# Performance work log

Measured on AMD Instinct MI355X. Metric: run time of the kernel, lower is better.

Reference implementation:

```python
import jax, jax.numpy as jnp
import numpy as np

LAMBDA_COLOR = 0.01
BLUR = 0.01          # geomloss blur
P = 2                # geomloss p
EPS_FINAL = BLUR ** P  # 1e-4
# Note: with scaling=1.2 (>1), geomloss's epsilon_schedule arange is empty, so
# eps_list = [diameter**p, blur**p] -> exactly two annealing stages.


def cost_matrix(x, y, lambda_color):
    # x: [B,N,6], y: [B,M,6]
    cx, col_x = x[..., :3], x[..., 3:]
    cy, col_y = y[..., :3], y[..., 3:]
    max_norm = jnp.max(jnp.linalg.norm(jnp.concatenate([cx, cy], axis=1), axis=-1))
    s = 1.0 / (max_norm + 1e-6)
    cxn, cyn = cx * s, cy * s
    coord = jnp.sum((cxn[:, :, None, :] - cyn[:, None, :, :]) ** 2, axis=-1)  # [B,N,M]
    col_x = jnp.clip(col_x, 0.0, 1.0)
    col_y = jnp.clip(col_y, 0.0, 1.0)
    col = jnp.sum((col_x[:, :, None, :] - col_y[:, None, :, :]) ** 2, axis=-1)
    return jnp.maximum(coord + lambda_color * col, 0.0)


def softmin(eps, C, h):
    # h: [B,M] = log_weights + potential/eps ; C: [B,N,M]
    return -eps * jax.nn.logsumexp(h[:, None, :] - C / eps, axis=2)  # [B,N]


def sinkhorn_distance(x, y, lambda_color):
    B, N, _ = x.shape
    M = y.shape[1]
    a_log = jnp.full((B, N), -np.log(N), dtype=x.dtype)
    b_log = jnp.full((B, M), -np.log(M), dtype=x.dtype)

    C_xy = cost_matrix(x, y, lambda_color)          # [B,N,M]
    C_yx = jnp.swapaxes(C_xy, 1, 2)                 # cost is symmetric in x<->y

    # diameter over raw 6-d features (geomloss max_diameter)
    pts = jnp.concatenate([x.reshape(-1, x.shape[-1]), y.reshape(-1, y.shape[-1])], axis=0)
    diameter = jnp.linalg.norm(pts.max(0) - pts.min(0))
    eps_list = (diameter ** P, jnp.asarray(EPS_FINAL, x.dtype))

    # Sinkhorn loop runs without gradient through the potentials (geomloss semantics)
    Cs_xy = jax.lax.stop_gradient(C_xy)
    Cs_yx = jax.lax.stop_gradient(C_yx)

    eps = eps_list[0]
    f = softmin(eps, Cs_xy, b_log)   # potential on x
    g = softmin(eps, Cs_yx, a_log)   # potential on y
    for eps in eps_list:
        ft = softmin(eps, Cs_xy, b_log + g / eps)
        gt = softmin(eps, Cs_yx, a_log + f / eps)
        f, g = 0.5 * (f + ft), 0.5 * (g + gt)

    # final extrapolation with gradient-carrying cost, detached dual potentials
    eps = eps_list[-1]
    f_new = softmin(eps, C_xy, b_log + jax.lax.stop_gradient(g) / eps)
    g_new = softmin(eps, C_yx, a_log + jax.lax.stop_gradient(f) / eps)

    # <a,f> + <b,g> with uniform weights
    ot = f_new.mean(axis=1) + g_new.mean(axis=1)   # [B]
    return ot.mean() * 10.0


def setup_inputs() -> dict:
    key = jax.random.key(0)
    kx, ky = jax.random.split(key)
    x = jax.random.normal(kx, (4, 4096, 6), dtype=jnp.float32)
    y = jax.random.normal(ky, (4, 4096, 6), dtype=jnp.float32)
    return {"x": x, "y": y}


def reference(x, y):
    return sinkhorn_distance(x, y, LAMBDA_COLOR)
```

## Files before the change

### kernel.cpp

```cpp
#include <hip/hip_runtime.h>

#define B_ 4
#define N_ 4096
#define ROWS (B_ * N_)
#define PTS_TOTAL (2 * ROWS)

#define LOG2E 1.4426950408889634f
#define LN2   0.6931471805599453f
#define EPS1  1e-4f
#define NEG_LOG2M (-12.0f)
#define EPS1LNM 8.317766166719343e-4f
#define ENC_STRIDE 32

typedef _Float16 h2 __attribute__((ext_vector_type(2)));
typedef _Float16 v8h __attribute__((ext_vector_type(8)));
typedef float f32x4 __attribute__((ext_vector_type(4)));

__device__ inline float fexp2(float x) { return __builtin_amdgcn_exp2f(x); }
__device__ inline float flog2(float x) { return __builtin_amdgcn_logf(x); }

__device__ inline unsigned fenc(float f) {
  unsigned u = __float_as_uint(f);
  return (u & 0x80000000u) ? ~u : (u | 0x80000000u);
}
__device__ inline float fdec(unsigned u) {
  return (u & 0x80000000u) ? __uint_as_float(u & 0x7fffffffu)
                           : __uint_as_float(~u);
}
__device__ inline unsigned pkh2(float a, float b) {
  h2 hv; hv.x = (_Float16)a; hv.y = (_Float16)b;
  return __builtin_bit_cast(unsigned, hv);
}
__device__ inline v8h bcv8(uint4 u) { return __builtin_bit_cast(v8h, u); }

__global__ void init_kernel(unsigned* enc, float* MOM) {
  int t = threadIdx.x;
  if (t < 13) enc[t * ENC_STRIDE] = 0u;
  if (t < 512) MOM[t] = 0.0f;
}

__global__ __launch_bounds__(256) void reduce_kernel(
    const float* __restrict__ x, const float* __restrict__ y,
    unsigned* __restrict__ enc) {
  int idx = blockIdx.x * 256 + threadIdx.x;
  bool isx = idx < ROWS;
  const float* p = (isx ? x : y) + (size_t)(isx ? idx : idx - ROWS) * 6;
  float d[6];
#pragma unroll
  for (int k = 0; k < 6; ++k) d[k] = p[k];
  unsigned e[13];
  e[0] = fenc(d[0] * d[0] + d[1] * d[1] + d[2] * d[2]);
#pragma unroll
  for (int k = 0; k < 6; ++k) {
    e[1 + k] = fenc(d[k]);
    e[7 + k] = fenc(-d[k]);
  }
#pragma unroll
  for (int off = 32; off > 0; off >>= 1) {
#pragma unroll
    for (int k = 0; k < 13; ++k) {
      unsigned o = (unsigned)__shfl_xor((int)e[k], off);
      e[k] = e[k] > o ? e[k] : o;
    }
  }
  __shared__ unsigned sh[4][13];
  int wave = threadIdx.x >> 6, lane = threadIdx.x & 63;
  if (lane == 0) {
#pragma unroll
    for (int k = 0; k < 13; ++k) sh[wave][k] = e[k];
  }
  __syncthreads();
  if (threadIdx.x < 13) {
    unsigned v = sh[0][threadIdx.x];
#pragma unroll
    for (int w = 1; w < 4; ++w) v = v > sh[w][threadIdx.x] ? v : sh[w][threadIdx.x];
    atomicMax(&enc[threadIdx.x * ENC_STRIDE], v);
  }
}

__global__ __launch_bounds__(256) void pack_kernel(
    const float* __restrict__ x, const float* __restrict__ y,
    float4* __restrict__ XP, uint4* __restrict__ AREC,
    uint4* __restrict__ BREC, const unsigned* __restrict__ enc,
    float* __restrict__ sc, float* __restrict__ MOM1) {
  int g = blockIdx.x * 256 + threadIdx.x;
  int side = g >> 14, local = g & (ROWS - 1), batch = local >> 12;
  float s = 1.0f / (sqrtf(fdec(enc[0])) + 1e-6f);
  float eps0 = 0.0f;
#pragma unroll
  for (int k = 0; k < 6; ++k) {
    float dd = fdec(enc[(1 + k) * ENC_STRIDE]) + fdec(enc[(7 + k) * ENC_STRIDE]);
    eps0 += dd * dd;
  }
  if (g == 0) sc[0] = eps0;

  const float* p = (side ? y : x) + (size_t)local * 6;
  float v[6];
  v[0] = p[0] * s; v[1] = p[1] * s; v[2] = p[2] * s;
  v[3] = 0.1f * fminf(fmaxf(p[3], 0.0f), 1.0f);
  v[4] = 0.1f * fminf(fmaxf(p[4], 0.0f), 1.0f);
  v[5] = 0.1f * fminf(fmaxf(p[5], 0.0f), 1.0f);
  float q = v[0]*v[0] + v[1]*v[1] + v[2]*v[2] + v[3]*v[3] + v[4]*v[4] + v[5]*v[5];
  XP[(size_t)g * 2]     = make_float4(v[0], v[1], v[2], v[3]);
  XP[(size_t)g * 2 + 1] = make_float4(v[4], v[5], q, 0.0f);
  unsigned w01 = pkh2(v[0], v[1]), w23 = pkh2(v[2], v[3]), w45 = pkh2(v[4], v[5]);
  AREC[g] = (uint4){w01, w23, w45, pkh2(1.0f, 0.0f)};
  BREC[g] = (uint4){w01, w23, w45, 0u};

  float w = fexp2(NEG_LOG2M - q * (LOG2E / eps0));
  float acc[28];
  acc[0] = w;
  int kk = 1;
#pragma unroll
  for (int d = 0; d < 6; ++d) acc[kk++] = w * v[d];
#pragma unroll
  for (int d = 0; d < 6; ++d) {
    float wv = w * v[d];
#pragma unroll
    for (int e = d; e < 6; ++e) acc[kk++] = wv * v[e];
  }
#pragma unroll
  for (int off = 32; off > 0; off >>= 1) {
#pragma unroll
    for (int k = 0; k < 28; ++k) acc[k] += __shfl_xor(acc[k], off);
  }
  __shared__ float sh[4][28];
  int wave = threadIdx.x >> 6, lane = threadIdx.x & 63;
  if (lane == 0) {
#pragma unroll
    for (int k = 0; k < 28; ++k) sh[wave][k] = acc[k];
  }
  __syncthreads();
  if (threadIdx.x < 28) {
    float vv = (sh[0][threadIdx.x] + sh[1][threadIdx.x]) +
               (sh[2][threadIdx.x] + sh[3][threadIdx.x]);
    atomicAdd(&MOM1[(side * 4 + batch) * 32 + threadIdx.x], vv);
  }
}

__device__ inline float taylor_f(const float* __restrict__ M, const float* v,
                                 float q, float eps0) {
  float sc2 = 2.0f * LOG2E / eps0;
  float p[6];
#pragma unroll
  for (int d = 0; d < 6; ++d) p[d] = v[d] * sc2;
  float t1 = 0.0f;
#pragma unroll
  for (int d = 0; d < 6; ++d) t1 += p[d] * M[1 + d];
  float t2 = 0.0f;
  int kk = 7;
#pragma unroll
  for (int d = 0; d < 6; ++d) {
#pragma unroll
    for (int e = d; e < 6; ++e) {
      float coef = (d == e) ? 1.0f : 2.0f;
      t2 += coef * p[d] * p[e] * M[kk];
      kk++;
    }
  }
  float S = M[0] + LN2 * t1 + (0.5f * LN2 * LN2) * t2;
  return q - eps0 * LN2 * flog2(S);
}

__global__ __launch_bounds__(256) void rows1_kernel(
    const float4* __restrict__ XP, const float* __restrict__ MOM1,
    float* __restrict__ MOM2, float* __restrict__ FG1,
    const float* __restrict__ sc) {
  int g = blockIdx.x * 256 + threadIdx.x;
  int side = g >> 14, local = g & (ROWS - 1), batch = local >> 12;
  float eps0 = sc[0];
  float4 a = XP[(size_t)g * 2], b = XP[(size_t)g * 2 + 1];
  float v[6] = {a.x, a.y, a.z, a.w, b.x, b.y};
  float q = b.z;
  const float* M = MOM1 + (((side ^ 1) * 4 + batch) * 32);
  float f1 = taylor_f(M, v, q, eps0);
  FG1[g] = f1;
  float w = fexp2(NEG_LOG2M + (f1 - q) * (LOG2E / eps0));
  float acc[28];
  acc[0] = w;
  int kk = 1;
#pragma unroll
  for (int d = 0; d < 6; ++d) acc[kk++] = w * v[d];
#pragma unroll
  for (int d = 0; d < 6; ++d) {
    float wv = w * v[d];
#pragma unroll
    for (int e = d; e < 6; ++e) acc[kk++] = wv * v[e];
  }
#pragma unroll
  for (int off = 32; off > 0; off >>= 1) {
#pragma unroll
    for (int k = 0; k < 28; ++k) acc[k] += __shfl_xor(acc[k], off);
  }
  __shared__ float sh[4][28];
  int wave = threadIdx.x >> 6, lane = threadIdx.x & 63;
  if (lane == 0) {
#pragma unroll
    for (int k = 0; k < 28; ++k) sh[wave][k] = acc[k];
  }
  __syncthreads();
  if (threadIdx.x < 28) {
    float vv = (sh[0][threadIdx.x] + sh[1][threadIdx.x]) +
               (sh[2][threadIdx.x] + sh[3][threadIdx.x]);
    atomicAdd(&MOM2[(side * 4 + batch) * 32 + threadIdx.x], vv);
  }
}

__global__ __launch_bounds__(256) void rows2_kernel(
    const float4* __restrict__ XP, const float* __restrict__ MOM2,
    const float* __restrict__ FG1, float* __restrict__ FG2,
    unsigned* __restrict__ BRECu, const float* __restrict__ sc) {
  int g = blockIdx.x * 256 + threadIdx.x;
  int side = g >> 14, local = g & (ROWS - 1), batch = local >> 12;
  float eps0 = sc[0];
  float4 a = XP[(size_t)g * 2], b = XP[(size_t)g * 2 + 1];
  float v[6] = {a.x, a.y, a.z, a.w, b.x, b.y};
  float q = b.z;
  const float* M = MOM2 + (((side ^ 1) * 4 + batch) * 32);
  float f_t = taylor_f(M, v, q, eps0);
  float f2v = 0.5f * (FG1[g] + f_t);
  FG2[g] = f2v;
  float hs2 = 0.5f * (f2v - q - EPS1LNM);
  BRECu[4 * g + 3] = pkh2(hs2, 0.0f);
}

__global__ __launch_bounds__(256) void softmax_pair_kernel(
    const uint4* __restrict__ AREC, const uint4* __restrict__ BIN,
    uint4* __restrict__ BOUT, const float* __restrict__ XPf,
    const float* __restrict__ prev, float* __restrict__ part) {
  int t = threadIdx.x;
  int wave = t >> 6, lane = t & 63;
  int l16 = lane & 15;
  bool ld = lane < 16;
  int grow0 = blockIdx.x * 32;
  int side = grow0 >> 14;
  int batch = (grow0 & (ROWS - 1)) >> 12;
  int colrec0 = (side ^ 1) * ROWS + batch * 4096 + wave * 1024;

  uint4 z4 = (uint4){0u, 0u, 0u, 0u};
  uint4 a1u = z4, a2u = z4;
  if (ld) {
    a1u = AREC[grow0 + l16];
    a2u = AREC[grow0 + 16 + l16];
  }
  v8h a1 = bcv8(a1u), a2 = bcv8(a2u);

  f32x4 m2a = {-3.0e38f, -3.0e38f, -3.0e38f, -3.0e38f};
  f32x4 m2b = m2a;
  const f32x4 cz = {0.0f, 0.0f, 0.0f, 0.0f};

#pragma unroll 4
  for (int tt = 0; tt < 64; ++tt) {
    uint4 bu = z4;
    if (ld) bu = BIN[colrec0 + tt * 16 + l16];
    v8h b = bcv8(bu);
    f32x4 d1 = __builtin_amdgcn_mfma_f32_16x16x32_f16(a1, b, cz, 0, 0, 0);
    f32x4 d2 = __builtin_amdgcn_mfma_f32_16x16x32_f16(a2, b, cz, 0, 0, 0);
    m2a = __builtin_elementwise_max(m2a, d1);
    m2b = __builtin_elementwise_max(m2b, d2);
  }

#pragma unroll
  for (int off = 1; off <= 8; off <<= 1) {
#pragma unroll
    for (int r = 0; r < 4; ++r) {
      m2a[r] = fmaxf(m2a[r], __shfl_xor(m2a[r], off));
      m2b[r] = fmaxf(m2b[r], __shfl_xor(m2b[r], off));
    }
  }

  __shared__ float lm[4][32];
  __shared__ float fsh[32];
  if (l16 == 0) {
    int qd = lane >> 4;
#pragma unroll
    for (int r = 0; r < 4; ++r) {
      lm[wave][qd * 4 + r] = m2a[r];
      lm[wave][16 + qd * 4 + r] = m2b[r];
    }
  }
  __syncthreads();
  if (t < 32) {
    int g = grow0 + t;
    float m = fmaxf(fmaxf(lm[0][t], lm[1][t]), fmaxf(lm[2][t], lm[3][t]));
    float q = XPf[(size_t)g * 8 + 6];
    float f_t = q - 2.0f * m;
    float fo = prev ? 0.5f * (prev[g] + f_t) : f_t;
    if (BOUT) {
      float hs = 0.5f * (fo - q - EPS1LNM);
      uint4 ar = AREC[g];
      BOUT[g] = (uint4){ar.x, ar.y, ar.z, pkh2(hs, 0.0f)};
    }
    if (part) {
      fsh[t] = fo;
      __builtin_amdgcn_s_waitcnt(0);
      if (t == 0) {
        float ssum = 0.0f;
#pragma unroll
        for (int k = 0; k < 32; ++k) ssum += fsh[k];
        part[blockIdx.x] = ssum;
      }
    }
  }
}

__global__ __launch_bounds__(256) void final_kernel(
    const float* __restrict__ part, float* __restrict__ out) {
  float acc = 0.0f;
  for (int i = threadIdx.x; i < 1024; i += 256) acc += part[i];
  __shared__ float sh[256];
  sh[threadIdx.x] = acc;
  __syncthreads();
  for (int st = 128; st > 0; st >>= 1) {
    if (threadIdx.x < st) sh[threadIdx.x] += sh[threadIdx.x + st];
    __syncthreads();
  }
  if (threadIdx.x == 0) out[0] = sh[0] * (10.0f / (float)ROWS);
}

extern "C" void kernel_launch(void* const* d_in, const int* in_sizes, int n_in,
                              void* d_out, int out_size, void* d_ws,
                              size_t ws_size, hipStream_t stream) {
  const float* x = (const float*)d_in[0];
  const float* y = (const float*)d_in[1];
  float* out = (float*)d_out;
  float* w = (float*)d_ws;
  unsigned* enc = (unsigned*)d_ws;
  float* sc   = w + 448;
  float* MOM  = w + 512;
  float* MOM1 = MOM;
  float* MOM2 = MOM + 256;
  float* base = w + 1024;
  float4* XP   = (float4*)base;
  uint4* AREC  = (uint4*)(base + 262144);
  uint4* BRECA = (uint4*)(base + 262144 + 131072);
  uint4* BRECB = (uint4*)(base + 262144 + 262144);
  float* FG1   = base + 262144 + 262144 + 131072;
  float* FG2   = FG1 + PTS_TOTAL;
  float* PART  = FG2 + PTS_TOTAL;

  init_kernel<<<1, 512, 0, stream>>>(enc, MOM);
  reduce_kernel<<<PTS_TOTAL / 256, 256, 0, stream>>>(x, y, enc);
  pack_kernel<<<PTS_TOTAL / 256, 256, 0, stream>>>(x, y, XP, AREC, BRECA, enc,
                                                   sc, MOM1);
  rows1_kernel<<<PTS_TOTAL / 256, 256, 0, stream>>>(XP, MOM1, MOM2, FG1, sc);
  rows2_kernel<<<PTS_TOTAL / 256, 256, 0, stream>>>(XP, MOM2, FG1, FG2,
                                                    (unsigned*)BRECA, sc);
  softmax_pair_kernel<<<1024, 256, 0, stream>>>(AREC, BRECA, BRECB,
                                                (const float*)XP, FG2, nullptr);
  softmax_pair_kernel<<<1024, 256, 0, stream>>>(AREC, BRECB, nullptr,
                                                (const float*)XP, nullptr, PART);
  final_kernel<<<1, 256, 0, stream>>>(PART, out);
}
```

Baseline: 118.0 us.

## Fuse all stages into one persistent kernel with software grid barriers

Replaces the chain of eight kernel launches with one 256-block persistent kernel that separates stages with atomic-counter grid barriers. Global max and moment reductions now go through per-block partial buffers, with no atomics into shared accumulators. Each block handles 128 rows and reuses 8 A fragments per B load in the MFMA max loop. The final sum is accumulated into the output by atomics. This removes launch overhead and intermediate buffers (XP, FG1/FG2). It assumes all 256 blocks are co-resident and spin-waits at each barrier, and the softmax phase now runs on only 256 blocks instead of 1024.

```diff
diff --git a/kernel.cpp b/kernel.cpp
--- a/kernel.cpp
+++ b/kernel.cpp
@@ -1,16 +1,13 @@
 #include <hip/hip_runtime.h>
 
-#define B_ 4
-#define N_ 4096
-#define ROWS (B_ * N_)
-#define PTS_TOTAL (2 * ROWS)
+#define ROWS 16384
+#define PTS_TOTAL 32768
+#define NBLK 256
 
 #define LOG2E 1.4426950408889634f
 #define LN2   0.6931471805599453f
-#define EPS1  1e-4f
 #define NEG_LOG2M (-12.0f)
 #define EPS1LNM 8.317766166719343e-4f
-#define ENC_STRIDE 32
 
 typedef _Float16 h2 __attribute__((ext_vector_type(2)));
 typedef _Float16 v8h __attribute__((ext_vector_type(8)));
@@ -18,128 +15,14 @@
 
 __device__ inline float fexp2(float x) { return __builtin_amdgcn_exp2f(x); }
 __device__ inline float flog2(float x) { return __builtin_amdgcn_logf(x); }
-
-__device__ inline unsigned fenc(float f) {
-  unsigned u = __float_as_uint(f);
-  return (u & 0x80000000u) ? ~u : (u | 0x80000000u);
-}
-__device__ inline float fdec(unsigned u) {
-  return (u & 0x80000000u) ? __uint_as_float(u & 0x7fffffffu)
-                           : __uint_as_float(~u);
-}
 __device__ inline unsigned pkh2(float a, float b) {
   h2 hv; hv.x = (_Float16)a; hv.y = (_Float16)b;
   return __builtin_bit_cast(unsigned, hv);
 }
 __device__ inline v8h bcv8(uint4 u) { return __builtin_bit_cast(v8h, u); }
 
-__global__ void init_kernel(unsigned* enc, float* MOM) {
-  int t = threadIdx.x;
-  if (t < 13) enc[t * ENC_STRIDE] = 0u;
-  if (t < 512) MOM[t] = 0.0f;
-}
-
-__global__ __launch_bounds__(256) void reduce_kernel(
-    const float* __restrict__ x, const float* __restrict__ y,
-    unsigned* __restrict__ enc) {
-  int idx = blockIdx.x * 256 + threadIdx.x;
-  bool isx = idx < ROWS;
-  const float* p = (isx ? x : y) + (size_t)(isx ? idx : idx - ROWS) * 6;
-  float d[6];
-#pragma unroll
-  for (int k = 0; k < 6; ++k) d[k] = p[k];
-  unsigned e[13];
-  e[0] = fenc(d[0] * d[0] + d[1] * d[1] + d[2] * d[2]);
-#pragma unroll
-  for (int k = 0; k < 6; ++k) {
-    e[1 + k] = fenc(d[k]);
-    e[7 + k] = fenc(-d[k]);
-  }
-#pragma unroll
-  for (int off = 32; off > 0; off >>= 1) {
-#pragma unroll
-    for (int k = 0; k < 13; ++k) {
-      unsigned o = (unsigned)__shfl_xor((int)e[k], off);
-      e[k] = e[k] > o ? e[k] : o;
-    }
-  }
-  __shared__ unsigned sh[4][13];
-  int wave = threadIdx.x >> 6, lane = threadIdx.x & 63;
-  if (lane == 0) {
-#pragma unroll
-    for (int k = 0; k < 13; ++k) sh[wave][k] = e[k];
-  }
-  __syncthreads();
-  if (threadIdx.x < 13) {
-    unsigned v = sh[0][threadIdx.x];
-#pragma unroll
-    for (int w = 1; w < 4; ++w) v = v > sh[w][threadIdx.x] ? v : sh[w][threadIdx.x];
-    atomicMax(&enc[threadIdx.x * ENC_STRIDE], v);
-  }
-}
-
-__global__ __launch_bounds__(256) void pack_kernel(
-    const float* __restrict__ x, const float* __restrict__ y,
-    float4* __restrict__ XP, uint4* __restrict__ AREC,
-    uint4* __restrict__ BREC, const unsigned* __restrict__ enc,
-    float* __restrict__ sc, float* __restrict__ MOM1) {
-  int g = blockIdx.x * 256 + threadIdx.x;
-  int side = g >> 14, local = g & (ROWS - 1), batch = local >> 12;
-  float s = 1.0f / (sqrtf(fdec(enc[0])) + 1e-6f);
-  float eps0 = 0.0f;
-#pragma unroll
-  for (int k = 0; k < 6; ++k) {
-    float dd = fdec(enc[(1 + k) * ENC_STRIDE]) + fdec(enc[(7 + k) * ENC_STRIDE]);
-    eps0 += dd * dd;
-  }
-  if (g == 0) sc[0] = eps0;
-
-  const float* p = (side ? y : x) + (size_t)local * 6;
-  float v[6];
-  v[0] = p[0] * s; v[1] = p[1] * s; v[2] = p[2] * s;
-  v[3] = 0.1f * fminf(fmaxf(p[3], 0.0f), 1.0f);
-  v[4] = 0.1f * fminf(fmaxf(p[4], 0.0f), 1.0f);
-  v[5] = 0.1f * fminf(fmaxf(p[5], 0.0f), 1.0f);
-  float q = v[0]*v[0] + v[1]*v[1] + v[2]*v[2] + v[3]*v[3] + v[4]*v[4] + v[5]*v[5];
-  XP[(size_t)g * 2]     = make_float4(v[0], v[1], v[2], v[3]);
-  XP[(size_t)g * 2 + 1] = make_float4(v[4], v[5], q, 0.0f);
-  unsigned w01 = pkh2(v[0], v[1]), w23 = pkh2(v[2], v[3]), w45 = pkh2(v[4], v[5]);
-  AREC[g] = (uint4){w01, w23, w45, pkh2(1.0f, 0.0f)};
-  BREC[g] = (uint4){w01, w23, w45, 0u};
-
-  float w = fexp2(NEG_LOG2M - q * (LOG2E / eps0));
-  float acc[28];
-  acc[0] = w;
-  int kk = 1;
-#pragma unroll
-  for (int d = 0; d < 6; ++d) acc[kk++] = w * v[d];
-#pragma unroll
-  for (int d = 0; d < 6; ++d) {
-    float wv = w * v[d];
-#pragma unroll
-    for (int e = d; e < 6; ++e) acc[kk++] = wv * v[e];
-  }
-#pragma unroll
-  for (int off = 32; off > 0; off >>= 1) {
-#pragma unroll
-    for (int k = 0; k < 28; ++k) acc[k] += __shfl_xor(acc[k], off);
-  }
-  __shared__ float sh[4][28];
-  int wave = threadIdx.x >> 6, lane = threadIdx.x & 63;
-  if (lane == 0) {
-#pragma unroll
-    for (int k = 0; k < 28; ++k) sh[wave][k] = acc[k];
-  }
-  __syncthreads();
-  if (threadIdx.x < 28) {
-    float vv = (sh[0][threadIdx.x] + sh[1][threadIdx.x]) +
-               (sh[2][threadIdx.x] + sh[3][threadIdx.x]);
-    atomicAdd(&MOM1[(side * 4 + batch) * 32 + threadIdx.x], vv);
-  }
-}
-
-__device__ inline float taylor_f(const float* __restrict__ M, const float* v,
-                                 float q, float eps0) {
+__device__ inline float taylor_f(const float* M, const float* v, float q,
+                                 float eps0) {
   float sc2 = 2.0f * LOG2E / eps0;
   float p[6];
 #pragma unroll
@@ -162,21 +45,7 @@
   return q - eps0 * LN2 * flog2(S);
 }
 
-__global__ __launch_bounds__(256) void rows1_kernel(
-    const float4* __restrict__ XP, const float* __restrict__ MOM1,
-    float* __restrict__ MOM2, float* __restrict__ FG1,
-    const float* __restrict__ sc) {
-  int g = blockIdx.x * 256 + threadIdx.x;
-  int side = g >> 14, local = g & (ROWS - 1), batch = local >> 12;
-  float eps0 = sc[0];
-  float4 a = XP[(size_t)g * 2], b = XP[(size_t)g * 2 + 1];
-  float v[6] = {a.x, a.y, a.z, a.w, b.x, b.y};
-  float q = b.z;
-  const float* M = MOM1 + (((side ^ 1) * 4 + batch) * 32);
-  float f1 = taylor_f(M, v, q, eps0);
-  FG1[g] = f1;
-  float w = fexp2(NEG_LOG2M + (f1 - q) * (LOG2E / eps0));
-  float acc[28];
+__device__ inline void mom_acc(float w, const float* v, float* acc) {
   acc[0] = w;
   int kk = 1;
 #pragma unroll
@@ -187,135 +56,248 @@
 #pragma unroll
     for (int e = d; e < 6; ++e) acc[kk++] = wv * v[e];
   }
-#pragma unroll
-  for (int off = 32; off > 0; off >>= 1) {
-#pragma unroll
-    for (int k = 0; k < 28; ++k) acc[k] += __shfl_xor(acc[k], off);
-  }
-  __shared__ float sh[4][28];
-  int wave = threadIdx.x >> 6, lane = threadIdx.x & 63;
-  if (lane == 0) {
-#pragma unroll
-    for (int k = 0; k < 28; ++k) sh[wave][k] = acc[k];
-  }
-  __syncthreads();
-  if (threadIdx.x < 28) {
-    float vv = (sh[0][threadIdx.x] + sh[1][threadIdx.x]) +
-               (sh[2][threadIdx.x] + sh[3][threadIdx.x]);
-    atomicAdd(&MOM2[(side * 4 + batch) * 32 + threadIdx.x], vv);
-  }
-}
-
-__global__ __launch_bounds__(256) void rows2_kernel(
-    const float4* __restrict__ XP, const float* __restrict__ MOM2,
-    const float* __restrict__ FG1, float* __restrict__ FG2,
-    unsigned* __restrict__ BRECu, const float* __restrict__ sc) {
-  int g = blockIdx.x * 256 + threadIdx.x;
-  int side = g >> 14, local = g & (ROWS - 1), batch = local >> 12;
-  float eps0 = sc[0];
-  float4 a = XP[(size_t)g * 2], b = XP[(size_t)g * 2 + 1];
-  float v[6] = {a.x, a.y, a.z, a.w, b.x, b.y};
-  float q = b.z;
-  const float* M = MOM2 + (((side ^ 1) * 4 + batch) * 32);
-  float f_t = taylor_f(M, v, q, eps0);
-  float f2v = 0.5f * (FG1[g] + f_t);
-  FG2[g] = f2v;
-  float hs2 = 0.5f * (f2v - q - EPS1LNM);
-  BRECu[4 * g + 3] = pkh2(hs2, 0.0f);
-}
-
-__global__ __launch_bounds__(256) void softmax_pair_kernel(
-    const uint4* __restrict__ AREC, const uint4* __restrict__ BIN,
-    uint4* __restrict__ BOUT, const float* __restrict__ XPf,
-    const float* __restrict__ prev, float* __restrict__ part) {
-  int t = threadIdx.x;
-  int wave = t >> 6, lane = t & 63;
-  int l16 = lane & 15;
-  bool ld = lane < 16;
-  int grow0 = blockIdx.x * 32;
-  int side = grow0 >> 14;
-  int batch = (grow0 & (ROWS - 1)) >> 12;
-  int colrec0 = (side ^ 1) * ROWS + batch * 4096 + wave * 1024;
-
-  uint4 z4 = (uint4){0u, 0u, 0u, 0u};
-  uint4 a1u = z4, a2u = z4;
-  if (ld) {
-    a1u = AREC[grow0 + l16];
-    a2u = AREC[grow0 + 16 + l16];
-  }
-  v8h a1 = bcv8(a1u), a2 = bcv8(a2u);
-
-  f32x4 m2a = {-3.0e38f, -3.0e38f, -3.0e38f, -3.0e38f};
-  f32x4 m2b = m2a;
+}
+
+__device__ inline void gbar(unsigned* cnt, unsigned* gen) {
+  __syncthreads();
+  if (threadIdx.x == 0) {
+    __threadfence();
+    unsigned g = __hip_atomic_load(gen, __ATOMIC_RELAXED,
+                                   __HIP_MEMORY_SCOPE_AGENT);
+    unsigned a = __hip_atomic_fetch_add(cnt, 1u, __ATOMIC_ACQ_REL,
+                                        __HIP_MEMORY_SCOPE_AGENT);
+    if (a == NBLK - 1) {
+      __hip_atomic_store(cnt, 0u, __ATOMIC_RELAXED, __HIP_MEMORY_SCOPE_AGENT);
+      __hip_atomic_fetch_add(gen, 1u, __ATOMIC_ACQ_REL,
+                             __HIP_MEMORY_SCOPE_AGENT);
+    } else {
+      while (__hip_atomic_load(gen, __ATOMIC_RELAXED,
+                               __HIP_MEMORY_SCOPE_AGENT) == g)
+        __builtin_amdgcn_s_sleep(1);
+    }
+    __threadfence();
+  }
+  __syncthreads();
+}
+
+__global__ void init_kernel(unsigned* bar, float* out) {
+  if (threadIdx.x == 0) { bar[0] = 0u; bar[1] = 0u; out[0] = 0.0f; }
+}
+
+__global__ __launch_bounds__(256, 2) void mega_kernel(
+    const float* __restrict__ x, const float* __restrict__ y,
+    float* __restrict__ out, unsigned* __restrict__ bar,
+    float* __restrict__ MAXP,
+    float* __restrict__ MOMP1,
+    float* __restrict__ MOMP2,
+    uint4* __restrict__ AREC, uint4* __restrict__ BRECA,
+    uint4* __restrict__ BRECB) {
+  const int t = threadIdx.x;
+  const int blk = blockIdx.x;
+  const int wave = t >> 6, lane = t & 63;
+  unsigned* cnt = bar;
+  unsigned* gen = bar + 1;
+
+  __shared__ float shred[2][28];
+  __shared__ float shfin[28];
+  __shared__ float lm[4][128];
+  __shared__ float ssum2[2];
+
+  const int idx = blk * 128 + t;
+  if (t < 128) {
+    bool isx = idx < ROWS;
+    const float* p = (isx ? x : y) + (size_t)(isx ? idx : idx - ROWS) * 6;
+    float d[6];
+#pragma unroll
+    for (int k = 0; k < 6; ++k) d[k] = p[k];
+    float e[13];
+    e[0] = d[0] * d[0] + d[1] * d[1] + d[2] * d[2];
+#pragma unroll
+    for (int k = 0; k < 6; ++k) {
+      e[1 + k] = d[k];
+      e[7 + k] = -d[k];
+    }
+#pragma unroll
+    for (int off = 32; off > 0; off >>= 1) {
+#pragma unroll
+      for (int k = 0; k < 13; ++k) e[k] = fmaxf(e[k], __shfl_xor(e[k], off));
+    }
+    if (lane == 0) {
+#pragma unroll
+      for (int k = 0; k < 13; ++k) shred[wave][k] = e[k];
+    }
+  }
+  __syncthreads();
+  if (t < 13) MAXP[t * NBLK + blk] = fmaxf(shred[0][t], shred[1][t]);
+  gbar(cnt, gen);
+
+  if (wave == 0) {
+    for (int k = 0; k < 13; ++k) {
+      float m = -3.0e38f;
+      for (int j = lane; j < NBLK; j += 64) m = fmaxf(m, MAXP[k * NBLK + j]);
+#pragma unroll
+      for (int off = 32; off > 0; off >>= 1) m = fmaxf(m, __shfl_xor(m, off));
+      if (lane == 0) shfin[k] = m;
+    }
+  }
+  __syncthreads();
+  float eps0 = 0.0f;
+  {
+    float acc = 0.0f;
+#pragma unroll
+    for (int k = 0; k < 6; ++k) {
+      float dd = shfin[1 + k] + shfin[7 + k];
+      acc += dd * dd;
+    }
+    eps0 = acc;
+  }
+  const float s = 1.0f / (sqrtf(shfin[0]) + 1e-6f);
+  __syncthreads();
+
+  float v[6] = {0, 0, 0, 0, 0, 0};
+  float q = 0.0f, f1 = 0.0f, f2v = 0.0f;
+  unsigned w01 = 0, w23 = 0, w45 = 0;
+  if (t < 128) {
+    bool isx = idx < ROWS;
+    int local = isx ? idx : idx - ROWS;
+    const float* p = (isx ? x : y) + (size_t)local * 6;
+    v[0] = p[0] * s; v[1] = p[1] * s; v[2] = p[2] * s;
+    v[3] = 0.1f * fminf(fmaxf(p[3], 0.0f), 1.0f);
+    v[4] = 0.1f * fminf(fmaxf(p[4], 0.0f), 1.0f);
+    v[5] = 0.1f * fminf(fmaxf(p[5], 0.0f), 1.0f);
+    q = v[0]*v[0] + v[1]*v[1] + v[2]*v[2] + v[3]*v[3] + v[4]*v[4] + v[5]*v[5];
+    w01 = pkh2(v[0], v[1]); w23 = pkh2(v[2], v[3]); w45 = pkh2(v[4], v[5]);
+    AREC[idx]  = (uint4){w01, w23, w45, pkh2(1.0f, 0.0f)};
+    BRECA[idx] = (uint4){w01, w23, w45, 0u};
+    float acc[28];
+    mom_acc(fexp2(NEG_LOG2M - q * (LOG2E / eps0)), v, acc);
+#pragma unroll
+    for (int off = 32; off > 0; off >>= 1) {
+#pragma unroll
+      for (int k = 0; k < 28; ++k) acc[k] += __shfl_xor(acc[k], off);
+    }
+    if (lane == 0) {
+#pragma unroll
+      for (int k = 0; k < 28; ++k) shred[wave][k] = acc[k];
+    }
+  }
+  __syncthreads();
+  if (t < 28) MOMP1[blk * 32 + t] = shred[0][t] + shred[1][t];
+  gbar(cnt, gen);
+
+  const int g0 = (blk >> 5) << 5;
+  if (t < 28) {
+    float ssum = 0.0f;
+    for (int b = g0; b < g0 + 32; ++b) ssum += MOMP1[b * 32 + t];
+    shfin[t] = ssum;
+  }
+  __syncthreads();
+  if (t < 128) {
+    f1 = taylor_f(shfin, v, q, eps0);
+    float acc[28];
+    mom_acc(fexp2(NEG_LOG2M + (f1 - q) * (LOG2E / eps0)), v, acc);
+#pragma unroll
+    for (int off = 32; off > 0; off >>= 1) {
+#pragma unroll
+      for (int k = 0; k < 28; ++k) acc[k] += __shfl_xor(acc[k], off);
+    }
+    if (lane == 0) {
+#pragma unroll
+      for (int k = 0; k < 28; ++k) shred[wave][k] = acc[k];
+    }
+  }
+  __syncthreads();
+  if (t < 28) MOMP2[blk * 32 + t] = shred[0][t] + shred[1][t];
+  gbar(cnt, gen);
+
+  if (t < 28) {
+    float ssum = 0.0f;
+    for (int b = g0; b < g0 + 32; ++b) ssum += MOMP2[b * 32 + t];
+    shfin[t] = ssum;
+  }
+  __syncthreads();
+  if (t < 128) {
+    float f_t = taylor_f(shfin, v, q, eps0);
+    f2v = 0.5f * (f1 + f_t);
+    ((unsigned*)BRECA)[4 * idx + 3] = pkh2(0.5f * (f2v - q - EPS1LNM), 0.0f);
+  }
+  gbar(cnt, gen);
+
+  const int grow0 = blk * 128;
+  const int mside = grow0 >> 14;
+  const int mbatch = (grow0 & (ROWS - 1)) >> 12;
+  const int colrec0 = (mside ^ 1) * ROWS + mbatch * 4096 + wave * 1024;
+  const int l16 = lane & 15;
+  const bool ld = lane < 16;
+  const uint4 z4 = (uint4){0u, 0u, 0u, 0u};
+  v8h a[8];
+#pragma unroll
+  for (int i = 0; i < 8; ++i) {
+    uint4 au = z4;
+    if (ld) au = AREC[grow0 + i * 16 + l16];
+    a[i] = bcv8(au);
+  }
   const f32x4 cz = {0.0f, 0.0f, 0.0f, 0.0f};
 
+#pragma unroll
+  for (int phase = 0; phase < 2; ++phase) {
+    const uint4* __restrict__ BIN = (phase == 0) ? BRECA : BRECB;
+    f32x4 m2[8];
+#pragma unroll
+    for (int i = 0; i < 8; ++i)
+      m2[i] = (f32x4){-3.0e38f, -3.0e38f, -3.0e38f, -3.0e38f};
 #pragma unroll 4
-  for (int tt = 0; tt < 64; ++tt) {
-    uint4 bu = z4;
-    if (ld) bu = BIN[colrec0 + tt * 16 + l16];
-    v8h b = bcv8(bu);
-    f32x4 d1 = __builtin_amdgcn_mfma_f32_16x16x32_f16(a1, b, cz, 0, 0, 0);
-    f32x4 d2 = __builtin_amdgcn_mfma_f32_16x16x32_f16(a2, b, cz, 0, 0, 0);
-    m2a = __builtin_elementwise_max(m2a, d1);
-    m2b = __builtin_elementwise_max(m2b, d2);
-  }
-
-#pragma unroll
-  for (int off = 1; off <= 8; off <<= 1) {
-#pragma unroll
-    for (int r = 0; r < 4; ++r) {
-      m2a[r] = fmaxf(m2a[r], __shfl_xor(m2a[r], off));
-      m2b[r] = fmaxf(m2b[r], __shfl_xor(m2b[r], off));
-    }
-  }
-
-  __shared__ float lm[4][32];
-  __shared__ float fsh[32];
-  if (l16 == 0) {
-    int qd = lane >> 4;
-#pragma unroll
-    for (int r = 0; r < 4; ++r) {
-      lm[wave][qd * 4 + r] = m2a[r];
-      lm[wave][16 + qd * 4 + r] = m2b[r];
-    }
-  }
-  __syncthreads();
-  if (t < 32) {
-    int g = grow0 + t;
-    float m = fmaxf(fmaxf(lm[0][t], lm[1][t]), fmaxf(lm[2][t], lm[3][t]));
-    float q = XPf[(size_t)g * 8 + 6];
-    float f_t = q - 2.0f * m;
-    float fo = prev ? 0.5f * (prev[g] + f_t) : f_t;
-    if (BOUT) {
-      float hs = 0.5f * (fo - q - EPS1LNM);
-      uint4 ar = AREC[g];
-      BOUT[g] = (uint4){ar.x, ar.y, ar.z, pkh2(hs, 0.0f)};
-    }
-    if (part) {
-      fsh[t] = fo;
-      __builtin_amdgcn_s_waitcnt(0);
-      if (t == 0) {
-        float ssum = 0.0f;
-#pragma unroll
-        for (int k = 0; k < 32; ++k) ssum += fsh[k];
-        part[blockIdx.x] = ssum;
-      }
-    }
-  }
-}
-
-__global__ __launch_bounds__(256) void final_kernel(
-    const float* __restrict__ part, float* __restrict__ out) {
-  float acc = 0.0f;
-  for (int i = threadIdx.x; i < 1024; i += 256) acc += part[i];
-  __shared__ float sh[256];
-  sh[threadIdx.x] = acc;
-  __syncthreads();
-  for (int st = 128; st > 0; st >>= 1) {
-    if (threadIdx.x < st) sh[threadIdx.x] += sh[threadIdx.x + st];
+    for (int tt = 0; tt < 64; ++tt) {
+      uint4 bu = z4;
+      if (ld) bu = BIN[colrec0 + tt * 16 + l16];
+      v8h b = bcv8(bu);
+#pragma unroll
+      for (int i = 0; i < 8; ++i) {
+        f32x4 d = __builtin_amdgcn_mfma_f32_16x16x32_f16(a[i], b, cz, 0, 0, 0);
+        m2[i] = __builtin_elementwise_max(m2[i], d);
+      }
+    }
+#pragma unroll
+    for (int off = 1; off <= 8; off <<= 1) {
+#pragma unroll
+      for (int i = 0; i < 8; ++i) {
+#pragma unroll
+        for (int r = 0; r < 4; ++r)
+          m2[i][r] = fmaxf(m2[i][r], __shfl_xor(m2[i][r], off));
+      }
+    }
     __syncthreads();
-  }
-  if (threadIdx.x == 0) out[0] = sh[0] * (10.0f / (float)ROWS);
+    if (l16 == 0) {
+      int qd = lane >> 4;
+#pragma unroll
+      for (int i = 0; i < 8; ++i) {
+#pragma unroll
+        for (int r = 0; r < 4; ++r) lm[wave][i * 16 + qd * 4 + r] = m2[i][r];
+      }
+    }
+    __syncthreads();
+    if (phase == 0) {
+      if (t < 128) {
+        float m = fmaxf(fmaxf(lm[0][t], lm[1][t]), fmaxf(lm[2][t], lm[3][t]));
+        float fo = 0.5f * (f2v + (q - 2.0f * m));
+        BRECB[idx] = (uint4){w01, w23, w45,
+                             pkh2(0.5f * (fo - q - EPS1LNM), 0.0f)};
+      }
+      gbar(cnt, gen);
+    } else {
+      float fo = 0.0f;
+      if (t < 128) {
+        float m = fmaxf(fmaxf(lm[0][t], lm[1][t]), fmaxf(lm[2][t], lm[3][t]));
+        fo = q - 2.0f * m;
+#pragma unroll
+        for (int off = 32; off > 0; off >>= 1) fo += __shfl_xor(fo, off);
+        if (lane == 0) ssum2[wave] = fo;
+      }
+      __syncthreads();
+      if (t == 0)
+        atomicAdd(out, (ssum2[0] + ssum2[1]) * (10.0f / (float)ROWS));
+    }
+  }
 }
 
 extern "C" void kernel_launch(void* const* d_in, const int* in_sizes, int n_in,
@@ -325,30 +307,16 @@
   const float* y = (const float*)d_in[1];
   float* out = (float*)d_out;
   float* w = (float*)d_ws;
-  unsigned* enc = (unsigned*)d_ws;
-  float* sc   = w + 448;
-  float* MOM  = w + 512;
-  float* MOM1 = MOM;
-  float* MOM2 = MOM + 256;
-  float* base = w + 1024;
-  float4* XP   = (float4*)base;
-  uint4* AREC  = (uint4*)(base + 262144);
-  uint4* BRECA = (uint4*)(base + 262144 + 131072);
-  uint4* BRECB = (uint4*)(base + 262144 + 262144);
-  float* FG1   = base + 262144 + 262144 + 131072;
-  float* FG2   = FG1 + PTS_TOTAL;
-  float* PART  = FG2 + PTS_TOTAL;
-
-  init_kernel<<<1, 512, 0, stream>>>(enc, MOM);
-  reduce_kernel<<<PTS_TOTAL / 256, 256, 0, stream>>>(x, y, enc);
-  pack_kernel<<<PTS_TOTAL / 256, 256, 0, stream>>>(x, y, XP, AREC, BRECA, enc,
-                                                   sc, MOM1);
-  rows1_kernel<<<PTS_TOTAL / 256, 256, 0, stream>>>(XP, MOM1, MOM2, FG1, sc);
-  rows2_kernel<<<PTS_TOTAL / 256, 256, 0, stream>>>(XP, MOM2, FG1, FG2,
-                                                    (unsigned*)BRECA, sc);
-  softmax_pair_kernel<<<1024, 256, 0, stream>>>(AREC, BRECA, BRECB,
-                                                (const float*)XP, FG2, nullptr);
-  softmax_pair_kernel<<<1024, 256, 0, stream>>>(AREC, BRECB, nullptr,
-                                                (const float*)XP, nullptr, PART);
-  final_kernel<<<1, 256, 0, stream>>>(PART, out);
-}
+  unsigned* bar = (unsigned*)d_ws;
+  float* MAXP  = w + 64;
+  float* MOMP1 = w + 4096;
+  float* MOMP2 = w + 12288;
+  float* base  = w + 32768;
+  uint4* AREC  = (uint4*)base;
+  uint4* BRECA = (uint4*)(base + 131072);
+  uint4* BRECB = (uint4*)(base + 262144);
+
+  init_kernel<<<1, 64, 0, stream>>>(bar, out);
+  mega_kernel<<<NBLK, 256, 0, stream>>>(x, y, out, bar, MAXP, MOMP1, MOMP2,
+                                        AREC, BRECA, BRECB);
+}
```

Result: slower. 246.4 us (+108.9%).
